# Performance work log

Hardware: AMD Instinct MI355X
Metric: run time of the kernel (lower is better)

The kernel has to match this reference:

```python
import jax, jax.numpy as jnp
import numpy as np

N_NODES = 100000
N_EDGES = 1600000
NUM_RELS = 200
NUM_BASES = 4
IN_FEAT = 20   # hardcoded by `view(-1, 1, 20)` in the torch source
OUT_FEAT = 20
SUBMAT_IN = IN_FEAT // NUM_BASES   # 5
SUBMAT_OUT = OUT_FEAT // NUM_BASES # 5


def setup_inputs() -> dict:
    key = jax.random.key(0)
    ks = jax.random.split(key, 9)
    return {
        "h": jax.random.normal(ks[0], (N_NODES, IN_FEAT), dtype=jnp.float32),
        "weight": jax.random.normal(ks[1], (NUM_RELS, NUM_BASES * SUBMAT_IN * SUBMAT_OUT), dtype=jnp.float32),
        "bias_term": jax.random.normal(ks[2], (NUM_RELS, OUT_FEAT), dtype=jnp.float32),
        "gate_weight": jax.random.normal(ks[3], (NUM_RELS, OUT_FEAT, 1), dtype=jnp.float32),
        "gate_bias": jax.random.normal(ks[4], (NUM_RELS, 1), dtype=jnp.float32),
        "loop_weight": jax.random.normal(ks[5], (IN_FEAT, OUT_FEAT), dtype=jnp.float32),
        "edge_src": jax.random.randint(ks[6], (N_EDGES,), 0, N_NODES, dtype=jnp.int32),
        "edge_dst": jax.random.randint(ks[7], (N_EDGES,), 0, N_NODES, dtype=jnp.int32),
        "etype": jax.random.randint(ks[8], (NUM_RELS,), 0, NUM_RELS, dtype=jnp.int32) if False else jax.random.randint(ks[8], (N_EDGES,), 0, NUM_RELS, dtype=jnp.int32),
    }


def reference(h, weight, bias_term, gate_weight, gate_bias, loop_weight, edge_src, edge_dst, etype):
    n_nodes = h.shape[0]
    # self-loop message (dropout=0.0 -> identity)
    loop_message = h @ loop_weight                                    # [N, out]
    # per-edge relation-indexed gathers
    W = weight[etype].reshape(-1, NUM_BASES, SUBMAT_IN, SUBMAT_OUT)   # [E, B, si, so]
    src = h[edge_src]                                                 # [E, in]
    node = src.reshape(-1, NUM_BASES, SUBMAT_IN)                      # [E, B, si]
    # block-diagonal small matmul
    msg = jnp.einsum('ebi,ebio->ebo', node, W).reshape(-1, OUT_FEAT)  # [E, out]
    # gate: sigmoid(<full src node, gate_weight_r> + gate_bias_r)
    gw = gate_weight[etype, :, 0]                                     # [E, out(=20=in)]
    gb = gate_bias[etype, 0]                                          # [E]
    gate = jax.nn.sigmoid(jnp.sum(src * gw, axis=-1) + gb)            # [E]
    msg = gate[:, None] * (msg + bias_term[etype])                    # [E, out]
    # scatter-sum aggregation to destination nodes (zero init for isolated nodes)
    agg = jax.ops.segment_sum(msg, edge_dst, num_segments=n_nodes)    # [N, out]
    return jax.nn.relu(agg + loop_message)
```

## Files before the change

### kernel.cpp

```cpp
#include <hip/hip_runtime.h>
#include <hip/hip_fp16.h>
#include <math.h>
#include <string.h>

#define IN_FEAT 20
#define OUT_FEAT 20
#define NUM_BASES 4
#define SUBMAT_IN 5
#define SUBMAT_OUT 5
#define NUM_RELS 200
#define CAP 64
#define NPB 160
#define BCAP 3072
#define EPB 8192
#define NBAT (EPB / 4096)


typedef _Float16 v2h __attribute__((ext_vector_type(2)));

__device__ __forceinline__ float fdot2u(unsigned a, __half2 b, float c) {
#if __has_builtin(__builtin_amdgcn_fdot2)
    union { unsigned u; v2h v; } ca; ca.u = a;
    union { __half2 h; v2h v; } cb; cb.h = b;
    return __builtin_amdgcn_fdot2(ca.v, cb.v, c, false);
#else
    union { unsigned u; __half2 h; } ca; ca.u = a;
    float2 fa = __half22float2(ca.h), fb = __half22float2(b);
    return fmaf(fa.x, fb.x, fmaf(fa.y, fb.y, c));
#endif
}

__device__ __forceinline__ __half2 u2h2(unsigned x) {
    union { unsigned u; __half2 h; } c; c.u = x; return c.h;
}

__global__ void __launch_bounds__(1024)
prep_kernel(const float* __restrict__ h, __half* __restrict__ h_pad,
            const int* __restrict__ edge_src,
            const int* __restrict__ edge_dst,
            const int* __restrict__ etype,
            int* __restrict__ cursor,
            unsigned* __restrict__ bucketed,
            int n_nodes, int n_edges, int nb, int nsb) {
    __shared__ int  lhist[640];
    __shared__ int  lofs[640];
    __shared__ int  lrank[640];
    __shared__ int  lbase[640];
    __shared__ int  lws[16];
    __shared__ unsigned img[EPB];
    __shared__ unsigned short bid[EPB];
    int tid = threadIdx.x;

    if (blockIdx.x >= nsb) {
        int v = (blockIdx.x - nsb) * 1024 + tid;
        if (v >= n_nodes) return;
        const float4* hp = (const float4*)(h + (size_t)v * IN_FEAT);
        float4 a = hp[0], b = hp[1], c = hp[2], d = hp[3], e = hp[4];
        __half2 p0 = __floats2half2_rn(a.x, c.z);
        __half2 p1 = __floats2half2_rn(a.y, c.w);
        __half2 p2 = __floats2half2_rn(a.z, d.x);
        __half2 p3 = __floats2half2_rn(a.w, d.y);
        __half2 p4 = __floats2half2_rn(b.x, d.z);
        __half2 p5 = __floats2half2_rn(b.y, d.w);
        __half2 p6 = __floats2half2_rn(b.z, e.x);
        __half2 p7 = __floats2half2_rn(b.w, e.y);
        __half2 p8 = __floats2half2_rn(c.x, e.z);
        __half2 p9 = __floats2half2_rn(c.y, e.w);
        uint2* dst = (uint2*)(h_pad + (size_t)v * 20);
        uint2 q0, q1, q2, q3, q4;
        q0.x = *(unsigned*)&p0; q0.y = *(unsigned*)&p1;
        q1.x = *(unsigned*)&p2; q1.y = *(unsigned*)&p3;
        q2.x = *(unsigned*)&p4; q2.y = *(unsigned*)&p5;
        q3.x = *(unsigned*)&p6; q3.y = *(unsigned*)&p7;
        q4.x = *(unsigned*)&p8; q4.y = *(unsigned*)&p9;
        dst[0] = q0; dst[1] = q1; dst[2] = q2; dst[3] = q3; dst[4] = q4;
        return;
    }

    for (int i = tid; i < nb; i += 1024) { lhist[i] = 0; lrank[i] = 0; }
    __syncthreads();

    int blockbase = blockIdx.x * EPB;
    int      dreg[NBAT * 4];
    unsigned upart[NBAT * 4];
#pragma unroll
    for (int bat = 0; bat < NBAT; ++bat) {
        int e0 = blockbase + bat * 4096 + tid * 4;
        if (e0 + 3 < n_edges) {
            int4 sv = *(const int4*)(edge_src + e0);
            int4 dv = *(const int4*)(edge_dst + e0);
            int4 tv = *(const int4*)(etype + e0);
            dreg[bat*4+0] = dv.x; upart[bat*4+0] = (unsigned)sv.x | ((unsigned)tv.x << 17);
            dreg[bat*4+1] = dv.y; upart[bat*4+1] = (unsigned)sv.y | ((unsigned)tv.y << 17);
            dreg[bat*4+2] = dv.z; upart[bat*4+2] = (unsigned)sv.z | ((unsigned)tv.z << 17);
            dreg[bat*4+3] = dv.w; upart[bat*4+3] = (unsigned)sv.w | ((unsigned)tv.w << 17);
            atomicAdd(&lhist[dv.x / NPB], 1);
            atomicAdd(&lhist[dv.y / NPB], 1);
            atomicAdd(&lhist[dv.z / NPB], 1);
            atomicAdd(&lhist[dv.w / NPB], 1);
        } else {
#pragma unroll
            for (int k = 0; k < 4; ++k) {
                int e = e0 + k;
                if (e < n_edges) {
                    int dk = edge_dst[e];
                    dreg[bat*4+k] = dk;
                    upart[bat*4+k] = (unsigned)edge_src[e] | ((unsigned)etype[e] << 17);
                    atomicAdd(&lhist[dk / NPB], 1);
                } else {
                    dreg[bat*4+k] = -1;
                }
            }
        }
    }
    __syncthreads();

    int hv = (tid < nb) ? lhist[tid] : 0;
    int x = hv;
#pragma unroll
    for (int s2 = 1; s2 < 64; s2 <<= 1) {
        int y = __shfl_up(x, s2, 64);
        if ((tid & 63) >= s2) x += y;
    }
    if ((tid & 63) == 63) lws[tid >> 6] = x;
    __syncthreads();
    if (tid < 16) {
        int w = lws[tid];
#pragma unroll
        for (int s2 = 1; s2 < 16; s2 <<= 1) {
            int y = __shfl_up(w, s2, 16);
            if (tid >= s2) w += y;
        }
        lws[tid] = w;
    }
    __syncthreads();
    int wb = (tid >> 6) ? lws[(tid >> 6) - 1] : 0;
    if (tid < nb) {
        lofs[tid] = wb + x - hv;
        if (hv > 0) lbase[tid] = atomicAdd(&cursor[tid], hv);
    }
    __syncthreads();

#pragma unroll
    for (int idx = 0; idx < NBAT * 4; ++idx) {
        int dk = dreg[idx];
        if (dk >= 0) {
            int bk = dk / NPB;
            int r = atomicAdd(&lrank[bk], 1);
            int dl = dk - bk * NPB;
            unsigned u = upart[idx] + ((unsigned)(dl * NUM_RELS) << 17);
            int pos = lofs[bk] + r;
            img[pos] = u;
            bid[pos] = (unsigned short)bk;
        }
    }
    __syncthreads();

    int m = n_edges - blockbase; if (m > EPB) m = EPB;
    for (int i = tid; i < m; i += 1024) {
        unsigned u = img[i];
        int b2 = (int)bid[i];
        int dst = lbase[b2] + (i - lofs[b2]);
        if (dst < BCAP) bucketed[(size_t)b2 * BCAP + dst] = u;
    }
}

__global__ void __launch_bounds__(1024)
place_csr_kernel(const int* __restrict__ cursor,
                 const unsigned* __restrict__ bucketed,
                 unsigned* __restrict__ records,
                 int* __restrict__ cnt,
                 int* __restrict__ off,
                 int n_nodes, int nb) {
    __shared__ unsigned simg[BCAP];
    __shared__ unsigned char sdl[BCAP];
    __shared__ int  rws[16];
    __shared__ int  pws[4];
    __shared__ int  lcnt[NPB];
    __shared__ int  sscan[NPB];
    __shared__ int  lrank[NPB];
    int b = blockIdx.x, tid = threadIdx.x;
    int node0 = b * NPB;

    int rv = (tid < b && tid < nb) ? min(cursor[tid], BCAP) : 0;
#pragma unroll
    for (int s2 = 32; s2 > 0; s2 >>= 1) rv += __shfl_xor(rv, s2, 64);
    if ((tid & 63) == 0) rws[tid >> 6] = rv;
    if (tid < NPB) { lcnt[tid] = 0; lrank[tid] = 0; }
    __syncthreads();
    if (tid == 0) {
        int s = 0;
#pragma unroll
        for (int k = 0; k < 16; ++k) s += rws[k];
        rws[0] = s;
    }
    __syncthreads();
    int gbase = rws[0];

    int m = cursor[b]; if (m > BCAP) m = BCAP;

    for (int i = tid; i < m; i += 1024) {
        unsigned u = bucketed[(size_t)b * BCAP + i];
        simg[i] = u;
        int dl = (int)((u >> 17) / NUM_RELS);
        sdl[i] = (unsigned char)dl;
        atomicAdd(&lcnt[dl], 1);
    }
    __syncthreads();

    int cv = (tid < NPB) ? lcnt[tid] : 0;
    int x = cv;
#pragma unroll
    for (int s2 = 1; s2 < 64; s2 <<= 1) {
        int y = __shfl_up(x, s2, 64);
        if ((tid & 63) >= s2) x += y;
    }
    if ((tid & 63) == 63 && (tid >> 6) < 3) pws[tid >> 6] = x;
    __syncthreads();
    if (tid < 4) {
        int w = (tid < 3) ? pws[tid] : 0;
#pragma unroll
        for (int s2 = 1; s2 < 4; s2 <<= 1) {
            int y = __shfl_up(w, s2, 4);
            if (tid >= s2) w += y;
        }
        pws[tid] = w;
    }
    __syncthreads();
    if (tid < NPB) {
        int wb = (tid >> 6) ? pws[(tid >> 6) - 1] : 0;
        int excl = wb + x - cv;
        int v = node0 + tid;
        if (v < n_nodes) { cnt[v] = cv; off[v] = gbase + excl; }
        sscan[tid] = excl;
    }
    __syncthreads();

    for (int i = tid; i < m; i += 1024) {
        unsigned u = simg[i];
        int dl = (int)sdl[i];
        int t = (int)(u >> 17) - dl * NUM_RELS;
        unsigned rec = (u & 0x1FFFFu) | ((unsigned)t << 17);
        int rk = atomicAdd(&lrank[dl], 1);
        records[(size_t)gbase + sscan[dl] + rk] = rec;
    }
}

__global__ void __launch_bounds__(1024, 4)
gather_kernel(const float* __restrict__ h,
              const __half* __restrict__ h_pad,
              const float* __restrict__ loop_weight,
              const float* __restrict__ weight,
              const float* __restrict__ bias_term,
              const float* __restrict__ gate_weight,
              const float* __restrict__ gate_bias,
              const int* __restrict__ cnt,
              const int* __restrict__ off,
              const unsigned* __restrict__ records,
              float* __restrict__ out, int n_nodes, int n_groups) {
    __shared__ __half2 lds_wp[NUM_RELS * 51];
    __shared__ __half2 lds_gw2[10 * 201];
    __shared__ __half2 lds_bt2[10 * 201];
    __shared__ float   lds_gb[NUM_RELS];
    __shared__ float   lds_lw[IN_FEAT * OUT_FEAT];
    int tid = threadIdx.x;
    for (int idx = tid; idx < NUM_RELS * 50; idx += 1024) {
        int t = idx / 50, f = idx - t * 50;
        lds_wp[t * 51 + f] = __floats2half2_rn(weight[t * 100 + f],
                                               weight[t * 100 + f + 50]);
    }
    for (int idx = tid; idx < 10 * NUM_RELS; idx += 1024) {
        int q = idx / NUM_RELS, t = idx - q * NUM_RELS;
        lds_gw2[q * 201 + t] = __floats2half2_rn(gate_weight[t * IN_FEAT + q],
                                                 gate_weight[t * IN_FEAT + q + 10]);
        lds_bt2[q * 201 + t] = __floats2half2_rn(bias_term[t * OUT_FEAT + q],
                                                 bias_term[t * OUT_FEAT + q + 10]);
    }
    for (int idx = tid; idx < NUM_RELS; idx += 1024) lds_gb[idx] = gate_bias[idx];
    for (int idx = tid; idx < IN_FEAT * OUT_FEAT; idx += 1024) lds_lw[idx] = loop_weight[idx];
    __syncthreads();

    int wave = blockIdx.x * 16 + (tid >> 6);
    int nwaves = gridDim.x * 16;
    int l = tid & 63;
    int l16 = l & 15;

    for (int grp = wave; grp < n_groups; grp += nwaves) {
        int v = grp * 4 + (l >> 4);
        bool valid = (v < n_nodes);
        int c = 0, base = 0;
        if (valid) { c = cnt[v]; base = off[v]; }
        if (c > CAP) c = CAP;

        float acc[OUT_FEAT];
#pragma unroll
        for (int j = 0; j < OUT_FEAT; ++j) acc[j] = 0.0f;

        if (valid) {
#pragma unroll
            for (int i0 = 0; i0 < 2; ++i0) {
                int i = l16 + i0 * 16;
                if (i < IN_FEAT) {
                    float s = h[(size_t)v * IN_FEAT + i];
#pragma unroll
                    for (int j = 0; j < OUT_FEAT; ++j)
                        acc[j] = fmaf(s, lds_lw[i * OUT_FEAT + j], acc[j]);
                }
            }
        }

#pragma unroll
        for (int it = 0; it < 4; ++it) {
            int slot = l16 + it * 16;
            if (valid && slot < c) {
                unsigned p = records[(size_t)base + slot];
                int srcid = (int)(p & 0x1FFFFu);
                int t = (int)(p >> 17);

                const uint2* sp = (const uint2*)(h_pad + (size_t)srcid * 20);
                uint2 A = sp[0], B = sp[1], C = sp[2], D = sp[3], E = sp[4];
                unsigned u[10] = {A.x, A.y, B.x, B.y, C.x, C.y, D.x, D.y, E.x, E.y};

                float g = lds_gb[t];
#pragma unroll
                for (int q = 0; q < 10; ++q)
                    g = fdot2u(u[q], lds_gw2[q * 201 + t], g);
                g = 1.0f / (1.0f + __expf(-g));
                __half2 g2 = __float2half2_rn(g);

                __half2 s2[10];
#pragma unroll
                for (int q = 0; q < 10; ++q) s2[q] = __hmul2(u2h2(u[q]), g2);

                __half2 m2[10];
#pragma unroll
                for (int q = 0; q < 10; ++q)
                    m2[q] = __hmul2(lds_bt2[q * 201 + t], g2);

                const __half2* wp = lds_wp + t * 51;
#pragma unroll
                for (int f = 0; f < 50; ++f) {
                    const int r  = f / 5;
                    const int o  = f - r * 5;
                    const int b0 = r / 5;
                    const int pp = b0 * 5 + o;
                    m2[pp] = __hfma2(s2[r], wp[f], m2[pp]);
                }

#pragma unroll
                for (int q = 0; q < 10; ++q) {
                    float2 fm = __half22float2(m2[q]);
                    acc[q]      += fm.x;
                    acc[q + 10] += fm.y;
                }
            }
        }

#pragma unroll
        for (int mask = 8; mask > 0; mask >>= 1) {
#pragma unroll
            for (int j = 0; j < OUT_FEAT; ++j)
                acc[j] += __shfl_xor(acc[j], mask, 16);
        }

        if (valid && l16 < OUT_FEAT / 4) {
            float4 tv;
            tv.x = fmaxf(acc[4 * l16 + 0], 0.0f);
            tv.y = fmaxf(acc[4 * l16 + 1], 0.0f);
            tv.z = fmaxf(acc[4 * l16 + 2], 0.0f);
            tv.w = fmaxf(acc[4 * l16 + 3], 0.0f);
            ((float4*)(out + (size_t)v * OUT_FEAT))[l16] = tv;
        }
    }
}

__global__ void loop_msg_kernel(const float* __restrict__ h,
                                const float* __restrict__ loop_weight,
                                float* __restrict__ out, int n_nodes) {
    int v = blockIdx.x * blockDim.x + threadIdx.x;
    if (v >= n_nodes) return;
    float src[IN_FEAT];
    const float4* hp = (const float4*)(h + (size_t)v * IN_FEAT);
#pragma unroll
    for (int i = 0; i < IN_FEAT / 4; ++i) {
        float4 t = hp[i];
        src[4 * i + 0] = t.x; src[4 * i + 1] = t.y;
        src[4 * i + 2] = t.z; src[4 * i + 3] = t.w;
    }
    float acc[OUT_FEAT];
#pragma unroll
    for (int j = 0; j < OUT_FEAT; ++j) acc[j] = 0.0f;
#pragma unroll
    for (int i = 0; i < IN_FEAT; ++i) {
        float s = src[i];
#pragma unroll
        for (int j = 0; j < OUT_FEAT; ++j)
            acc[j] = fmaf(s, loop_weight[i * OUT_FEAT + j], acc[j]);
    }
    float4* op = (float4*)(out + (size_t)v * OUT_FEAT);
#pragma unroll
    for (int j = 0; j < OUT_FEAT / 4; ++j) {
        float4 t;
        t.x = acc[4 * j + 0]; t.y = acc[4 * j + 1];
        t.z = acc[4 * j + 2]; t.w = acc[4 * j + 3];
        op[j] = t;
    }
}

__global__ void edge_atomic_kernel(const float* __restrict__ h,
                                   const float* __restrict__ weight,
                                   const float* __restrict__ bias_term,
                                   const float* __restrict__ gate_weight,
                                   const float* __restrict__ gate_bias,
                                   const int* __restrict__ edge_src,
                                   const int* __restrict__ edge_dst,
                                   const int* __restrict__ etype,
                                   float* __restrict__ out, int n_edges) {
    int e = blockIdx.x * blockDim.x + threadIdx.x;
    if (e >= n_edges) return;
    int s = edge_src[e], d = edge_dst[e], t = etype[e];
    float src[IN_FEAT];
    const float4* hp = (const float4*)(h + (size_t)s * IN_FEAT);
#pragma unroll
    for (int i = 0; i < IN_FEAT / 4; ++i) {
        float4 v = hp[i];
        src[4 * i + 0] = v.x; src[4 * i + 1] = v.y;
        src[4 * i + 2] = v.z; src[4 * i + 3] = v.w;
    }
    const float* W = weight + (size_t)t * 100;
    float msg[OUT_FEAT];
#pragma unroll
    for (int j = 0; j < OUT_FEAT; ++j) msg[j] = 0.0f;
#pragma unroll
    for (int b = 0; b < NUM_BASES; ++b)
#pragma unroll
        for (int i = 0; i < SUBMAT_IN; ++i) {
            float sv = src[b * SUBMAT_IN + i];
#pragma unroll
            for (int o = 0; o < SUBMAT_OUT; ++o)
                msg[b * SUBMAT_OUT + o] =
                    fmaf(sv, W[(b * SUBMAT_IN + i) * SUBMAT_OUT + o],
                         msg[b * SUBMAT_OUT + o]);
        }
    const float* gw = gate_weight + (size_t)t * OUT_FEAT;
    float g = gate_bias[t];
#pragma unroll
    for (int i = 0; i < IN_FEAT; ++i) g = fmaf(src[i], gw[i], g);
    g = 1.0f / (1.0f + __expf(-g));
    const float* bt = bias_term + (size_t)t * OUT_FEAT;
    float* dstp = out + (size_t)d * OUT_FEAT;
#pragma unroll
    for (int j = 0; j < OUT_FEAT; ++j) atomicAdd(&dstp[j], g * (msg[j] + bt[j]));
}

__global__ void relu_kernel(float* __restrict__ out, int n4) {
    int i = blockIdx.x * blockDim.x + threadIdx.x;
    if (i >= n4) return;
    float4* p = (float4*)out;
    float4 v = p[i];
    v.x = fmaxf(v.x, 0.0f); v.y = fmaxf(v.y, 0.0f);
    v.z = fmaxf(v.z, 0.0f); v.w = fmaxf(v.w, 0.0f);
    p[i] = v;
}

extern "C" void kernel_launch(void* const* d_in, const int* in_sizes, int n_in,
                              void* d_out, int out_size, void* d_ws, size_t ws_size,
                              hipStream_t stream) {
    const float* h           = (const float*)d_in[0];
    const float* weight      = (const float*)d_in[1];
    const float* bias_term   = (const float*)d_in[2];
    const float* gate_weight = (const float*)d_in[3];
    const float* gate_bias   = (const float*)d_in[4];
    const float* loop_weight = (const float*)d_in[5];
    const int* edge_src      = (const int*)d_in[6];
    const int* edge_dst      = (const int*)d_in[7];
    const int* etype         = (const int*)d_in[8];
    float* out = (float*)d_out;

    const int n_nodes = in_sizes[0] / IN_FEAT;
    const int n_edges = in_sizes[6];
    const int nb = (n_nodes + NPB - 1) / NPB;
    const int nsb = (n_edges + EPB - 1) / EPB;
    const int hb = (n_nodes + 1023) / 1024;

    size_t off_cursor   = 0;
    size_t off_bucketed = (((size_t)nb * 4 + 127) / 128) * 128;
    size_t off_records  = ((off_bucketed + (size_t)nb * BCAP * 4 + 127) / 128) * 128;
    size_t off_cnt      = ((off_records + (size_t)n_edges * 4 + 127) / 128) * 128;
    size_t off_offs     = ((off_cnt + (size_t)n_nodes * 4 + 127) / 128) * 128;
    size_t off_hpad     = ((off_offs + (size_t)n_nodes * 4 + 127) / 128) * 128;
    size_t need = off_hpad + (size_t)n_nodes * 40;

    bool ok = (ws_size >= need) && (n_nodes <= (1 << 17)) && (nb <= 1024) &&
              (in_sizes[4] == NUM_RELS) && (in_sizes[1] == NUM_RELS * 100) &&
              (in_sizes[5] == IN_FEAT * OUT_FEAT);

    if (ok) {
        int*  cursor      = (int*)((char*)d_ws + off_cursor);
        unsigned* bucketed = (unsigned*)((char*)d_ws + off_bucketed);
        unsigned* records = (unsigned*)((char*)d_ws + off_records);
        int*  cnt         = (int*)((char*)d_ws + off_cnt);
        int*  off         = (int*)((char*)d_ws + off_offs);
        __half* h_pad     = (__half*)((char*)d_ws + off_hpad);

        hipMemsetAsync(cursor, 0, (size_t)nb * sizeof(int), stream);
        prep_kernel<<<nsb + hb, 1024, 0, stream>>>(
            h, h_pad, edge_src, edge_dst, etype, cursor, bucketed,
            n_nodes, n_edges, nb, nsb);
        place_csr_kernel<<<nb, 1024, 0, stream>>>(
            cursor, bucketed, records, cnt, off, n_nodes, nb);
        int n_groups = (n_nodes + 3) / 4;
        gather_kernel<<<512, 1024, 0, stream>>>(
            h, h_pad, loop_weight, weight, bias_term, gate_weight, gate_bias,
            cnt, off, records, out, n_nodes, n_groups);
    } else {
        loop_msg_kernel<<<(n_nodes + 255) / 256, 256, 0, stream>>>(
            h, loop_weight, out, n_nodes);
        edge_atomic_kernel<<<(n_edges + 255) / 256, 256, 0, stream>>>(
            h, weight, bias_term, gate_weight, gate_bias,
            edge_src, edge_dst, etype, out, n_edges);
        relu_kernel<<<(n_nodes * OUT_FEAT / 4 + 255) / 256, 256, 0, stream>>>(
            out, n_nodes * OUT_FEAT / 4);
    }
}
```

Measured before the change: 179.5 us.

## Fuse CSR placement into gather kernel using per-block LDS records

Merges the CSR placement kernel into the gather kernel. Each block of 160 destination nodes now counts, scans and places its bucketed edge records into shared memory, then processes its own nodes straight from LDS. This removes one kernel launch and the global round trip of records, cnt and off. In exchange, every one of the ~625 blocks reloads and converts the relation weight tables into LDS. The larger LDS footprint may also lower occupancy, and bucketed is read twice from global memory.

```diff
diff --git a/kernel.cpp b/kernel.cpp
--- a/kernel.cpp
+++ b/kernel.cpp
@@ -165,105 +165,31 @@
     }
 }
 
-__global__ void __launch_bounds__(1024)
-place_csr_kernel(const int* __restrict__ cursor,
-                 const unsigned* __restrict__ bucketed,
-                 unsigned* __restrict__ records,
-                 int* __restrict__ cnt,
-                 int* __restrict__ off,
-                 int n_nodes, int nb) {
-    __shared__ unsigned simg[BCAP];
-    __shared__ unsigned char sdl[BCAP];
-    __shared__ int  rws[16];
-    __shared__ int  pws[4];
-    __shared__ int  lcnt[NPB];
-    __shared__ int  sscan[NPB];
-    __shared__ int  lrank[NPB];
-    int b = blockIdx.x, tid = threadIdx.x;
-    int node0 = b * NPB;
-
-    int rv = (tid < b && tid < nb) ? min(cursor[tid], BCAP) : 0;
-#pragma unroll
-    for (int s2 = 32; s2 > 0; s2 >>= 1) rv += __shfl_xor(rv, s2, 64);
-    if ((tid & 63) == 0) rws[tid >> 6] = rv;
-    if (tid < NPB) { lcnt[tid] = 0; lrank[tid] = 0; }
-    __syncthreads();
-    if (tid == 0) {
-        int s = 0;
-#pragma unroll
-        for (int k = 0; k < 16; ++k) s += rws[k];
-        rws[0] = s;
-    }
-    __syncthreads();
-    int gbase = rws[0];
-
-    int m = cursor[b]; if (m > BCAP) m = BCAP;
-
-    for (int i = tid; i < m; i += 1024) {
-        unsigned u = bucketed[(size_t)b * BCAP + i];
-        simg[i] = u;
-        int dl = (int)((u >> 17) / NUM_RELS);
-        sdl[i] = (unsigned char)dl;
-        atomicAdd(&lcnt[dl], 1);
-    }
-    __syncthreads();
-
-    int cv = (tid < NPB) ? lcnt[tid] : 0;
-    int x = cv;
-#pragma unroll
-    for (int s2 = 1; s2 < 64; s2 <<= 1) {
-        int y = __shfl_up(x, s2, 64);
-        if ((tid & 63) >= s2) x += y;
-    }
-    if ((tid & 63) == 63 && (tid >> 6) < 3) pws[tid >> 6] = x;
-    __syncthreads();
-    if (tid < 4) {
-        int w = (tid < 3) ? pws[tid] : 0;
-#pragma unroll
-        for (int s2 = 1; s2 < 4; s2 <<= 1) {
-            int y = __shfl_up(w, s2, 4);
-            if (tid >= s2) w += y;
-        }
-        pws[tid] = w;
-    }
-    __syncthreads();
-    if (tid < NPB) {
-        int wb = (tid >> 6) ? pws[(tid >> 6) - 1] : 0;
-        int excl = wb + x - cv;
-        int v = node0 + tid;
-        if (v < n_nodes) { cnt[v] = cv; off[v] = gbase + excl; }
-        sscan[tid] = excl;
-    }
-    __syncthreads();
-
-    for (int i = tid; i < m; i += 1024) {
-        unsigned u = simg[i];
-        int dl = (int)sdl[i];
-        int t = (int)(u >> 17) - dl * NUM_RELS;
-        unsigned rec = (u & 0x1FFFFu) | ((unsigned)t << 17);
-        int rk = atomicAdd(&lrank[dl], 1);
-        records[(size_t)gbase + sscan[dl] + rk] = rec;
-    }
-}
-
 __global__ void __launch_bounds__(1024, 4)
-gather_kernel(const float* __restrict__ h,
-              const __half* __restrict__ h_pad,
-              const float* __restrict__ loop_weight,
-              const float* __restrict__ weight,
-              const float* __restrict__ bias_term,
-              const float* __restrict__ gate_weight,
-              const float* __restrict__ gate_bias,
-              const int* __restrict__ cnt,
-              const int* __restrict__ off,
-              const unsigned* __restrict__ records,
-              float* __restrict__ out, int n_nodes, int n_groups) {
+place_gather_kernel(const float* __restrict__ h,
+                    const __half* __restrict__ h_pad,
+                    const float* __restrict__ loop_weight,
+                    const float* __restrict__ weight,
+                    const float* __restrict__ bias_term,
+                    const float* __restrict__ gate_weight,
+                    const float* __restrict__ gate_bias,
+                    const int* __restrict__ cursor,
+                    const unsigned* __restrict__ bucketed,
+                    float* __restrict__ out, int n_nodes) {
     __shared__ __half2 lds_wp[NUM_RELS * 51];
     __shared__ __half2 lds_gw2[10 * 201];
     __shared__ __half2 lds_bt2[10 * 201];
     __shared__ float   lds_gb[NUM_RELS];
     __shared__ float   lds_lw[IN_FEAT * OUT_FEAT];
+    __shared__ unsigned srec[BCAP];
+    __shared__ int     lcnt[NPB];
+    __shared__ int     sscan[NPB];
+    __shared__ int     lrank[NPB];
+    __shared__ int     pws[4];
     int tid = threadIdx.x;
+    int b = blockIdx.x;
+    int node0 = b * NPB;
+
     for (int idx = tid; idx < NUM_RELS * 50; idx += 1024) {
         int t = idx / 50, f = idx - t * 50;
         lds_wp[t * 51 + f] = __floats2half2_rn(weight[t * 100 + f],
@@ -278,19 +204,65 @@
     }
     for (int idx = tid; idx < NUM_RELS; idx += 1024) lds_gb[idx] = gate_bias[idx];
     for (int idx = tid; idx < IN_FEAT * OUT_FEAT; idx += 1024) lds_lw[idx] = loop_weight[idx];
-    __syncthreads();
-
-    int wave = blockIdx.x * 16 + (tid >> 6);
-    int nwaves = gridDim.x * 16;
+    if (tid < NPB) { lcnt[tid] = 0; lrank[tid] = 0; }
+    __syncthreads();
+
+    int m = cursor[b]; if (m > BCAP) m = BCAP;
+
+    for (int i = tid; i < m; i += 1024) {
+        unsigned u = bucketed[(size_t)b * BCAP + i];
+        int dl = (int)((u >> 17) / NUM_RELS);
+        atomicAdd(&lcnt[dl], 1);
+    }
+    __syncthreads();
+
+    int cv = (tid < NPB) ? lcnt[tid] : 0;
+    int x = cv;
+#pragma unroll
+    for (int s2 = 1; s2 < 64; s2 <<= 1) {
+        int y = __shfl_up(x, s2, 64);
+        if ((tid & 63) >= s2) x += y;
+    }
+    if ((tid & 63) == 63 && (tid >> 6) < 3) pws[tid >> 6] = x;
+    __syncthreads();
+    if (tid < 4) {
+        int w = (tid < 3) ? pws[tid] : 0;
+#pragma unroll
+        for (int s2 = 1; s2 < 4; s2 <<= 1) {
+            int y = __shfl_up(w, s2, 4);
+            if (tid >= s2) w += y;
+        }
+        pws[tid] = w;
+    }
+    __syncthreads();
+    if (tid < NPB) {
+        int wb = (tid >> 6) ? pws[(tid >> 6) - 1] : 0;
+        sscan[tid] = wb + x - cv;
+    }
+    __syncthreads();
+
+    for (int i = tid; i < m; i += 1024) {
+        unsigned u = bucketed[(size_t)b * BCAP + i];
+        int dl = (int)((u >> 17) / NUM_RELS);
+        int t = (int)(u >> 17) - dl * NUM_RELS;
+        unsigned rec = (u & 0x1FFFFu) | ((unsigned)t << 17);
+        int rk = atomicAdd(&lrank[dl], 1);
+        srec[sscan[dl] + rk] = rec;
+    }
+    __syncthreads();
+
+    int wave = tid >> 6;
     int l = tid & 63;
     int l16 = l & 15;
-
-    for (int grp = wave; grp < n_groups; grp += nwaves) {
-        int v = grp * 4 + (l >> 4);
+    int sub = l >> 4;
+
+    for (int grp = wave; grp < NPB / 4; grp += 16) {
+        int vl = grp * 4 + sub;
+        int v = node0 + vl;
         bool valid = (v < n_nodes);
-        int c = 0, base = 0;
-        if (valid) { c = cnt[v]; base = off[v]; }
+        int c = valid ? lcnt[vl] : 0;
         if (c > CAP) c = CAP;
+        int base = valid ? sscan[vl] : 0;
 
         float acc[OUT_FEAT];
 #pragma unroll
@@ -313,7 +285,7 @@
         for (int it = 0; it < 4; ++it) {
             int slot = l16 + it * 16;
             if (valid && slot < c) {
-                unsigned p = records[(size_t)base + slot];
+                unsigned p = srec[base + slot];
                 int srcid = (int)(p & 0x1FFFFu);
                 int t = (int)(p >> 17);
 
@@ -485,10 +457,7 @@
 
     size_t off_cursor   = 0;
     size_t off_bucketed = (((size_t)nb * 4 + 127) / 128) * 128;
-    size_t off_records  = ((off_bucketed + (size_t)nb * BCAP * 4 + 127) / 128) * 128;
-    size_t off_cnt      = ((off_records + (size_t)n_edges * 4 + 127) / 128) * 128;
-    size_t off_offs     = ((off_cnt + (size_t)n_nodes * 4 + 127) / 128) * 128;
-    size_t off_hpad     = ((off_offs + (size_t)n_nodes * 4 + 127) / 128) * 128;
+    size_t off_hpad     = ((off_bucketed + (size_t)nb * BCAP * 4 + 127) / 128) * 128;
     size_t need = off_hpad + (size_t)n_nodes * 40;
 
     bool ok = (ws_size >= need) && (n_nodes <= (1 << 17)) && (nb <= 1024) &&
@@ -498,21 +467,15 @@
     if (ok) {
         int*  cursor      = (int*)((char*)d_ws + off_cursor);
         unsigned* bucketed = (unsigned*)((char*)d_ws + off_bucketed);
-        unsigned* records = (unsigned*)((char*)d_ws + off_records);
-        int*  cnt         = (int*)((char*)d_ws + off_cnt);
-        int*  off         = (int*)((char*)d_ws + off_offs);
         __half* h_pad     = (__half*)((char*)d_ws + off_hpad);
 
         hipMemsetAsync(cursor, 0, (size_t)nb * sizeof(int), stream);
         prep_kernel<<<nsb + hb, 1024, 0, stream>>>(
             h, h_pad, edge_src, edge_dst, etype, cursor, bucketed,
             n_nodes, n_edges, nb, nsb);
-        place_csr_kernel<<<nb, 1024, 0, stream>>>(
-            cursor, bucketed, records, cnt, off, n_nodes, nb);
-        int n_groups = (n_nodes + 3) / 4;
-        gather_kernel<<<512, 1024, 0, stream>>>(
+        place_gather_kernel<<<nb, 1024, 0, stream>>>(
             h, h_pad, loop_weight, weight, bias_term, gate_weight, gate_bias,
-            cnt, off, records, out, n_nodes, n_groups);
+            cursor, bucketed, out, n_nodes);
     } else {
         loop_msg_kernel<<<(n_nodes + 255) / 256, 256, 0, stream>>>(
             h, loop_weight, out, n_nodes);
```

Result: no change. 177.5 us (-1.1%).
